# Kernel tuning notes

Measured on AMD Instinct MI355X. Metric: run time of the kernel, lower is better.

## Reference

```python
import jax, jax.numpy as jnp
import numpy as np

N_NODES = 1_000_000
N_EDGES = 16_000_000
D = 2          # num_dimensions (hard-coded in source)
H = 64         # hidden_channnels
G = 1024       # number of graphs in the batch


def setup_inputs() -> dict:
    key = jax.random.key(0)
    ks = jax.random.split(key, 10)
    x = jax.random.normal(ks[0], (N_NODES, D), dtype=jnp.float32)
    edge_index = jax.random.randint(ks[1], (2, N_EDGES), 0, N_NODES, dtype=jnp.int64)
    batch = jnp.sort(jax.random.randint(ks[2], (N_NODES,), 0, G, dtype=jnp.int64))
    s = 0.5
    return {
        "x": x,
        "lin_w": jax.random.normal(ks[3], (D, D), dtype=jnp.float32) * s,
        "lin_b": jnp.zeros((D,), jnp.float32),
        "gn_weight": jnp.ones((D,), jnp.float32),
        "gn_bias": jnp.zeros((D,), jnp.float32),
        "gn_mean_scale": jnp.ones((D,), jnp.float32),
        "gcn_w": jax.random.normal(ks[4], (D, D), dtype=jnp.float32) * s,
        "gcn_b": jnp.zeros((D,), jnp.float32),
        "fc1_w": jax.random.normal(ks[5], (H, D), dtype=jnp.float32) * s,
        "fc1_b": jnp.zeros((H,), jnp.float32),
        "fc2_w": jax.random.normal(ks[6], (D, H), dtype=jnp.float32) * (1.0 / np.sqrt(H)),
        "fc2_b": jnp.zeros((D,), jnp.float32),
        "edge_index": edge_index,
        "batch": batch,
    }


def reference(x, lin_w, lin_b, gn_weight, gn_bias, gn_mean_scale,
              gcn_w, gcn_b, fc1_w, fc1_b, fc2_w, fc2_b, edge_index, batch):
    n = x.shape[0]
    # lin
    h = x @ lin_w.T + lin_b
    # GraphNorm called without batch -> single-graph stats; eps = num_dimensions = 2 (arg-order quirk)
    mean = h.mean(axis=0)
    out = h - mean * gn_mean_scale
    var = (out * out).mean(axis=0)
    h = gn_weight * out * jax.lax.rsqrt(var + jnp.float32(D)) + gn_bias
    h = jax.nn.relu(h)
    # GCNConv (add_self_loops=True, sym norm) + residual
    row, col = edge_index[0], edge_index[1]
    deg = jax.ops.segment_sum(jnp.ones_like(col, dtype=h.dtype), col, num_segments=n) + 1.0
    dis = jax.lax.rsqrt(deg)                       # deg^{-1/2}
    hw = h @ gcn_w.T                               # [N, D]
    msg = (dis[row] * dis[col])[:, None] * hw[row] # [E, D]
    agg = jax.ops.segment_sum(msg, col, num_segments=n)
    conv = agg + hw / deg[:, None] + gcn_b         # self-loop term = dis_i^2 * hw_i
    h = conv + h
    # fc1
    h = h @ fc1_w.T + fc1_b                        # [N, H]
    # InstanceNorm1d on 2D input -> unbatched (C=N, L=H): per-row norm over H; eps = H (arg-order quirk)
    m = h.mean(axis=1, keepdims=True)
    v = ((h - m) ** 2).mean(axis=1, keepdims=True)
    h = (h - m) * jax.lax.rsqrt(v + jnp.float32(H))
    # fc2
    h = h @ fc2_w.T + fc2_b                        # [N, D]
    # scatter_mean over batch
    ssum = jax.ops.segment_sum(h, batch, num_segments=G)
    cnt = jax.ops.segment_sum(jnp.ones((n,), h.dtype), batch, num_segments=G)
    return ssum / jnp.maximum(cnt, 1.0)[:, None]
```

## Files before the change

kernel.cpp:

```cpp
#include <hip/hip_runtime.h>

#define BLK 256
#define CH 8192
#define BSHIFT 12
#define BRANGE 4096
#define BMASK 4095
#define NSB 512


__global__ void k_stats(const float* __restrict__ x, int n, double* __restrict__ partials) {
    float s0 = 0.f, s1 = 0.f, s2 = 0.f, s3 = 0.f, s4 = 0.f;
    int nv = n >> 1;
    int stride = gridDim.x * blockDim.x;
    for (int i = blockIdx.x * blockDim.x + threadIdx.x; i < nv; i += stride) {
        float4 v = reinterpret_cast<const float4*>(x)[i];
        s0 += v.x + v.z; s1 += v.y + v.w;
        s2 += v.x * v.x + v.z * v.z;
        s3 += v.y * v.y + v.w * v.w;
        s4 += v.x * v.y + v.z * v.w;
    }
    if (blockIdx.x == 0 && threadIdx.x == 0 && (n & 1)) {
        float2 v = reinterpret_cast<const float2*>(x)[n - 1];
        s0 += v.x; s1 += v.y; s2 += v.x * v.x; s3 += v.y * v.y; s4 += v.x * v.y;
    }
    for (int off = 32; off; off >>= 1) {
        s0 += __shfl_down(s0, off);
        s1 += __shfl_down(s1, off);
        s2 += __shfl_down(s2, off);
        s3 += __shfl_down(s3, off);
        s4 += __shfl_down(s4, off);
    }
    __shared__ double lds[4][5];
    int wid = threadIdx.x >> 6;
    if ((threadIdx.x & 63) == 0) {
        lds[wid][0] = s0; lds[wid][1] = s1; lds[wid][2] = s2;
        lds[wid][3] = s3; lds[wid][4] = s4;
    }
    __syncthreads();
    if (threadIdx.x == 0) {
        double t0 = 0, t1 = 0, t2 = 0, t3 = 0, t4 = 0;
        for (int w = 0; w < 4; ++w) {
            t0 += lds[w][0]; t1 += lds[w][1]; t2 += lds[w][2];
            t3 += lds[w][3]; t4 += lds[w][4];
        }
        double* o = partials + (size_t)blockIdx.x * 5;
        o[0] = t0; o[1] = t1; o[2] = t2; o[3] = t3; o[4] = t4;
    }
}


__global__ void k_params(const double* __restrict__ partials, int np,
                         const int* __restrict__ bhist, int NB,
                         int* __restrict__ gbase, int* __restrict__ cursor,
                         const float* lin_w, const float* lin_b,
                         const float* gn_w, const float* gn_b, const float* gn_ms,
                         const float* gcn_w, const float* gcn_b,
                         const float* fc1_w, const float* fc1_b,
                         const float* fc2_w, const float* fc2_b,
                         int n, float* __restrict__ P) {
    int tid = threadIdx.x;
    if (bhist) {
        __shared__ int si[256];
        int hv = (tid < NB) ? bhist[tid] : 0;
        si[tid] = hv; __syncthreads();
        for (int off = 1; off < 256; off <<= 1) {
            int t = (tid >= off) ? si[tid - off] : 0;
            __syncthreads();
            si[tid] += t;
            __syncthreads();
        }
        if (tid < NB) { gbase[tid] = si[tid] - hv; cursor[tid] = si[tid] - hv; }
        if (tid == 0) gbase[NB] = si[255];
        __syncthreads();
    }
    double a0 = 0, a1 = 0, a2 = 0, a3 = 0, a4 = 0;
    for (int i = tid; i < np; i += blockDim.x) {
        const double* q = partials + (size_t)i * 5;
        a0 += q[0]; a1 += q[1]; a2 += q[2]; a3 += q[3]; a4 += q[4];
    }
    for (int off = 32; off; off >>= 1) {
        a0 += __shfl_down(a0, off);
        a1 += __shfl_down(a1, off);
        a2 += __shfl_down(a2, off);
        a3 += __shfl_down(a3, off);
        a4 += __shfl_down(a4, off);
    }
    __shared__ double red[4][5];
    int wid = tid >> 6;
    if ((tid & 63) == 0) {
        red[wid][0] = a0; red[wid][1] = a1; red[wid][2] = a2;
        red[wid][3] = a3; red[wid][4] = a4;
    }
    __syncthreads();
    if (tid != 0) return;
    double Sx0 = 0, Sx1 = 0, Sxx = 0, Syy = 0, Sxy = 0;
    for (int w = 0; w < 4; ++w) {
        Sx0 += red[w][0]; Sx1 += red[w][1]; Sxx += red[w][2];
        Syy += red[w][3]; Sxy += red[w][4];
    }
    double N = (double)n;
    for (int c = 0; c < 2; ++c) {
        double L0 = lin_w[c * 2], L1 = lin_w[c * 2 + 1], lb = lin_b[c];
        double m   = (L0 * Sx0 + L1 * Sx1) / N + lb;
        double Eh2 = (L0 * L0 * Sxx + L1 * L1 * Syy + 2.0 * L0 * L1 * Sxy
                      + 2.0 * lb * (L0 * Sx0 + L1 * Sx1)) / N + lb * lb;
        double s   = gn_ms[c];
        double var = Eh2 - 2.0 * s * m * m + s * s * m * m;
        double inv = 1.0 / sqrt(var + 2.0);
        double gam = gn_w[c];
        P[c * 2 + 0] = (float)(gam * inv * L0);
        P[c * 2 + 1] = (float)(gam * inv * L1);
        P[4 + c]     = (float)(gam * inv * (lb - m * s) + gn_b[c]);
    }
    P[6] = gcn_w[0]; P[7] = gcn_w[1]; P[8] = gcn_w[2]; P[9] = gcn_w[3];
    P[10] = gcn_b[0]; P[11] = gcn_b[1];
    double b0 = 0, b1 = 0, bb = 0;
    for (int j = 0; j < 64; ++j) { b0 += fc1_w[2 * j]; b1 += fc1_w[2 * j + 1]; bb += fc1_b[j]; }
    b0 /= 64.0; b1 /= 64.0; bb /= 64.0;
    double S00 = 0, S01 = 0, S11 = 0, Sb0 = 0, Sb1 = 0, Sbb = 0;
    double M00 = 0, M01 = 0, M10 = 0, M11 = 0, t0 = 0, t1 = 0;
    for (int j = 0; j < 64; ++j) {
        double w0 = fc1_w[2 * j] - b0, w1 = fc1_w[2 * j + 1] - b1, b = fc1_b[j] - bb;
        S00 += w0 * w0; S01 += w0 * w1; S11 += w1 * w1;
        Sb0 += w0 * b;  Sb1 += w1 * b;  Sbb += b * b;
        double f0 = fc2_w[j], f1 = fc2_w[64 + j];
        M00 += f0 * w0; M01 += f0 * w1; t0 += f0 * b;
        M10 += f1 * w0; M11 += f1 * w1; t1 += f1 * b;
    }
    P[12] = (float)(S00 / 64.0); P[13] = (float)(S01 / 64.0); P[14] = (float)(S11 / 64.0);
    P[15] = (float)(Sb0 / 64.0); P[16] = (float)(Sb1 / 64.0); P[17] = (float)(Sbb / 64.0);
    P[18] = (float)M00; P[19] = (float)M01; P[20] = (float)M10; P[21] = (float)M11;
    P[22] = (float)t0;  P[23] = (float)t1;
    P[24] = fc2_b[0];   P[25] = fc2_b[1];
}


__global__ void k_hist(const int* __restrict__ col, int E, int NB, int* __restrict__ bhist) {
    __shared__ int h[256];
    for (int j = threadIdx.x; j < 256; j += blockDim.x) h[j] = 0;
    __syncthreads();
    int nq = E >> 2;
    int stride = gridDim.x * blockDim.x;
    for (int q = blockIdx.x * blockDim.x + threadIdx.x; q < nq; q += stride) {
        int4 c = reinterpret_cast<const int4*>(col)[q];
        atomicAdd(&h[c.x >> BSHIFT], 1);
        atomicAdd(&h[c.y >> BSHIFT], 1);
        atomicAdd(&h[c.z >> BSHIFT], 1);
        atomicAdd(&h[c.w >> BSHIFT], 1);
    }
    if (blockIdx.x == 0) {
        for (int e = (nq << 2) + threadIdx.x; e < E; e += blockDim.x)
            atomicAdd(&h[col[e] >> BSHIFT], 1);
    }
    __syncthreads();
    for (int j = threadIdx.x; j < NB; j += blockDim.x)
        if (h[j]) atomicAdd(&bhist[j], h[j]);
}

__global__ __launch_bounds__(256) void k_binA(const int* __restrict__ row,
                                              const int* __restrict__ col, int E,
                                              int NB, int* __restrict__ cursor,
                                              unsigned* __restrict__ staging) {
    __shared__ unsigned buf[CH];
    __shared__ int h[256], si[256], lpos[256], lcur[256];
    int tid = threadIdx.x;
    int start = blockIdx.x * CH;
    int end = start + CH; if (end > E) end = E;
    h[tid] = 0;
    __syncthreads();
    for (int e = start + tid; e < end; e += 256)
        atomicAdd(&h[col[e] >> BSHIFT], 1);
    __syncthreads();
    int hv = h[tid];
    si[tid] = hv; __syncthreads();
    for (int off = 1; off < 256; off <<= 1) {
        int t = (tid >= off) ? si[tid - off] : 0;
        __syncthreads();
        si[tid] += t;
        __syncthreads();
    }
    lpos[tid] = si[tid] - hv;
    lcur[tid] = (tid < NB && hv) ? atomicAdd(&cursor[tid], hv) : 0;
    __syncthreads();
    for (int e = start + tid; e < end; e += 256) {
        int c = col[e];
        unsigned w = ((unsigned)row[e] << BSHIFT) | (unsigned)(c & BMASK);
        int slot = atomicAdd(&lpos[c >> BSHIFT], 1);
        buf[slot] = w;
    }
    __syncthreads();
    int wid = tid >> 6, lane = tid & 63;
    for (int b = wid; b < NB; b += 4) {
        int m = h[b];
        if (!m) continue;
        int lb = si[b] - m;
        int g = lcur[b];
        for (int k = lane; k < m; k += 64)
            staging[g + k] = buf[lb + k];
    }
}

__global__ __launch_bounds__(1024) void k_degprep(const unsigned* __restrict__ staging,
                                                  const int* __restrict__ gbase,
                                                  const float* __restrict__ x,
                                                  const float* __restrict__ P,
                                                  int n, int* __restrict__ deg,
                                                  float2* __restrict__ p) {
    __shared__ int hist[BRANGE];
    int tid = threadIdx.x;
    for (int j = tid; j < BRANGE; j += 1024) hist[j] = 0;
    __syncthreads();
    int s = gbase[blockIdx.x], e = gbase[blockIdx.x + 1];
    int pre = (4 - (s & 3)) & 3; int cnt = e - s; if (pre > cnt) pre = cnt;
    for (int i = s + tid; i < s + pre; i += 1024)
        atomicAdd(&hist[staging[i] & BMASK], 1);
    int vs = s + pre;
    int nq = (e - vs) >> 2;
    const uint4* sv = reinterpret_cast<const uint4*>(staging + vs);
    for (int q = tid; q < nq; q += 1024) {
        uint4 w = sv[q];
        atomicAdd(&hist[w.x & BMASK], 1);
        atomicAdd(&hist[w.y & BMASK], 1);
        atomicAdd(&hist[w.z & BMASK], 1);
        atomicAdd(&hist[w.w & BMASK], 1);
    }
    for (int i = vs + (nq << 2) + tid; i < e; i += 1024)
        atomicAdd(&hist[staging[i] & BMASK], 1);
    __syncthreads();
    float A00 = P[0], A01 = P[1], A10 = P[2], A11 = P[3], q0 = P[4], q1 = P[5];
    float g00 = P[6], g01 = P[7], g10 = P[8], g11 = P[9];
    int nb = blockIdx.x << BSHIFT;
    int lim = n - nb; if (lim > BRANGE) lim = BRANGE;
    for (int j = tid; j < lim; j += 1024) {
        int d = hist[j];
        deg[nb + j] = d;
        float2 v = reinterpret_cast<const float2*>(x)[nb + j];
        float gg0 = fmaxf(fmaf(A00, v.x, fmaf(A01, v.y, q0)), 0.f);
        float gg1 = fmaxf(fmaf(A10, v.x, fmaf(A11, v.y, q1)), 0.f);
        float hw0 = g00 * gg0 + g01 * gg1;
        float hw1 = g10 * gg0 + g11 * gg1;
        float degf = (float)d + 1.0f;
        float dis = rsqrtf(degf);
        p[nb + j] = make_float2(dis * hw0, dis * hw1);
    }
}

__global__ void k_aggB(const unsigned* __restrict__ staging, const int* __restrict__ gbase,
                       const float2* __restrict__ p, int n, float2* __restrict__ agg) {
    __shared__ float acc[2 * BRANGE];
    for (int j = threadIdx.x; j < 2 * BRANGE; j += blockDim.x) acc[j] = 0.f;
    __syncthreads();
    int s = gbase[blockIdx.x], e = gbase[blockIdx.x + 1];
    int cnt = e - s;
    int pre = (4 - (s & 3)) & 3; if (pre > cnt) pre = cnt;
    for (int i = s + threadIdx.x; i < s + pre; i += blockDim.x) {
        unsigned w = staging[i]; float2 pv = p[w >> BSHIFT];
        atomicAdd(&acc[2 * (w & BMASK)],     pv.x);
        atomicAdd(&acc[2 * (w & BMASK) + 1], pv.y);
    }
    int vs = s + pre;
    int nq = (e - vs) >> 2;
    const uint4* sv = reinterpret_cast<const uint4*>(staging + vs);
    #pragma unroll 4
    for (int q = threadIdx.x; q < nq; q += blockDim.x) {
        uint4 w = sv[q];
        float2 p0 = p[w.x >> BSHIFT], p1 = p[w.y >> BSHIFT];
        float2 p2 = p[w.z >> BSHIFT], p3 = p[w.w >> BSHIFT];
        atomicAdd(&acc[2 * (w.x & BMASK)],     p0.x);
        atomicAdd(&acc[2 * (w.x & BMASK) + 1], p0.y);
        atomicAdd(&acc[2 * (w.y & BMASK)],     p1.x);
        atomicAdd(&acc[2 * (w.y & BMASK) + 1], p1.y);
        atomicAdd(&acc[2 * (w.z & BMASK)],     p2.x);
        atomicAdd(&acc[2 * (w.z & BMASK) + 1], p2.y);
        atomicAdd(&acc[2 * (w.w & BMASK)],     p3.x);
        atomicAdd(&acc[2 * (w.w & BMASK) + 1], p3.y);
    }
    for (int i = vs + (nq << 2) + threadIdx.x; i < e; i += blockDim.x) {
        unsigned w = staging[i]; float2 pv = p[w >> BSHIFT];
        atomicAdd(&acc[2 * (w & BMASK)],     pv.x);
        atomicAdd(&acc[2 * (w & BMASK) + 1], pv.y);
    }
    __syncthreads();
    int nb = blockIdx.x << BSHIFT;
    for (int j = threadIdx.x; j < BRANGE && nb + j < n; j += blockDim.x)
        agg[nb + j] = make_float2(acc[2 * j], acc[2 * j + 1]);
}


__global__ void k_final(const float* __restrict__ x, const int* __restrict__ deg,
                        const float* __restrict__ agg, const int* __restrict__ batch,
                        const float* __restrict__ P, int n,
                        float* __restrict__ gsum, float* __restrict__ gcnt) {
    int i = blockIdx.x * blockDim.x + threadIdx.x;
    bool valid = i < n;
    float A00 = P[0], A01 = P[1], A10 = P[2], A11 = P[3], q0 = P[4], q1 = P[5];
    float g00 = P[6], g01 = P[7], g10 = P[8], g11 = P[9];
    float gb0 = P[10], gb1 = P[11];
    float S00 = P[12], S01 = P[13], S11 = P[14], Sb0 = P[15], Sb1 = P[16], Sbb = P[17];
    float M00 = P[18], M01 = P[19], M10 = P[20], M11 = P[21];
    float t0 = P[22], t1 = P[23], fb0 = P[24], fb1 = P[25];

    float o0 = 0.f, o1 = 0.f;
    int b = 0;
    if (valid) {
        float2 v = reinterpret_cast<const float2*>(x)[i];
        float g0 = fmaxf(fmaf(A00, v.x, fmaf(A01, v.y, q0)), 0.f);
        float g1 = fmaxf(fmaf(A10, v.x, fmaf(A11, v.y, q1)), 0.f);
        float hw0 = g00 * g0 + g01 * g1;
        float hw1 = g10 * g0 + g11 * g1;
        float degf = (float)deg[i] + 1.0f;
        float dis = rsqrtf(degf);
        float a0 = agg[2 * i], a1 = agg[2 * i + 1];
        float c0 = dis * a0 + hw0 / degf + gb0 + g0;
        float c1 = dis * a1 + hw1 / degf + gb1 + g1;
        float vq = S00 * c0 * c0 + 2.f * S01 * c0 * c1 + S11 * c1 * c1
                 + 2.f * Sb0 * c0 + 2.f * Sb1 * c1 + Sbb;
        float inv = rsqrtf(vq + 64.0f);
        o0 = inv * (M00 * c0 + M01 * c1 + t0) + fb0;
        o1 = inv * (M10 * c0 + M11 * c1 + t1) + fb1;
        b = batch[i];
    }
    unsigned long long act = __ballot(valid);
    if (act == ~0ull) {
        int b0 = __shfl(b, 0);
        if (__all(b == b0)) {
            float s0 = o0, s1 = o1;
            for (int off = 32; off; off >>= 1) {
                s0 += __shfl_down(s0, off);
                s1 += __shfl_down(s1, off);
            }
            if ((threadIdx.x & 63) == 0) {
                atomicAdd(&gsum[2 * b0], s0);
                atomicAdd(&gsum[2 * b0 + 1], s1);
                atomicAdd(&gcnt[b0], 64.0f);
            }
        } else {
            atomicAdd(&gsum[2 * b], o0);
            atomicAdd(&gsum[2 * b + 1], o1);
            atomicAdd(&gcnt[b], 1.0f);
        }
    } else if (valid) {
        atomicAdd(&gsum[2 * b], o0);
        atomicAdd(&gsum[2 * b + 1], o1);
        atomicAdd(&gcnt[b], 1.0f);
    }
}

__global__ void k_div(const float* __restrict__ gsum, const float* __restrict__ gcnt,
                      float* __restrict__ out, int G) {
    int g = blockIdx.x * blockDim.x + threadIdx.x;
    if (g < G) {
        float c = fmaxf(gcnt[g], 1.0f);
        out[2 * g]     = gsum[2 * g] / c;
        out[2 * g + 1] = gsum[2 * g + 1] / c;
    }
}


__global__ void k_prep(const float* __restrict__ x, const int* __restrict__ deg,
                       const float* __restrict__ P, int n, float2* __restrict__ p) {
    int stride = gridDim.x * blockDim.x;
    float A00 = P[0], A01 = P[1], A10 = P[2], A11 = P[3], q0 = P[4], q1 = P[5];
    float g00 = P[6], g01 = P[7], g10 = P[8], g11 = P[9];
    for (int i = blockIdx.x * blockDim.x + threadIdx.x; i < n; i += stride) {
        float2 v = reinterpret_cast<const float2*>(x)[i];
        float g0 = fmaxf(fmaf(A00, v.x, fmaf(A01, v.y, q0)), 0.f);
        float g1 = fmaxf(fmaf(A10, v.x, fmaf(A11, v.y, q1)), 0.f);
        float hw0 = g00 * g0 + g01 * g1;
        float hw1 = g10 * g0 + g11 * g1;
        float degf = (float)deg[i] + 1.0f;
        float dis = rsqrtf(degf);
        p[i] = make_float2(dis * hw0, dis * hw1);
    }
}

__global__ void k_deg(const int* __restrict__ col, int E, int* __restrict__ deg) {
    int nq = (E + 3) >> 2;
    int q = blockIdx.x * blockDim.x + threadIdx.x;
    if (q >= nq) return;
    int base = q << 2;
    if (base + 3 < E) {
        int4 c = reinterpret_cast<const int4*>(col)[q];
        atomicAdd(&deg[c.x], 1); atomicAdd(&deg[c.y], 1);
        atomicAdd(&deg[c.z], 1); atomicAdd(&deg[c.w], 1);
    } else {
        for (int e = base; e < E; ++e) atomicAdd(&deg[col[e]], 1);
    }
}

__global__ void k_edge(const int* __restrict__ row, const int* __restrict__ col, int E,
                       const float2* __restrict__ p, float* __restrict__ agg) {
    int nq = (E + 3) >> 2;
    int q = blockIdx.x * blockDim.x + threadIdx.x;
    if (q >= nq) return;
    int base = q << 2;
    if (base + 3 < E) {
        int4 r = reinterpret_cast<const int4*>(row)[q];
        int4 c = reinterpret_cast<const int4*>(col)[q];
        float2 p0 = p[r.x], p1 = p[r.y], p2 = p[r.z], p3 = p[r.w];
        atomicAdd(&agg[2 * c.x], p0.x); atomicAdd(&agg[2 * c.x + 1], p0.y);
        atomicAdd(&agg[2 * c.y], p1.x); atomicAdd(&agg[2 * c.y + 1], p1.y);
        atomicAdd(&agg[2 * c.z], p2.x); atomicAdd(&agg[2 * c.z + 1], p2.y);
        atomicAdd(&agg[2 * c.w], p3.x); atomicAdd(&agg[2 * c.w + 1], p3.y);
    } else {
        for (int e = base; e < E; ++e) {
            float2 pv = p[row[e]];
            atomicAdd(&agg[2 * col[e]], pv.x);
            atomicAdd(&agg[2 * col[e] + 1], pv.y);
        }
    }
}


extern "C" void kernel_launch(void* const* d_in, const int* in_sizes, int n_in,
                              void* d_out, int out_size, void* d_ws, size_t ws_size,
                              hipStream_t stream) {
    const float* x      = (const float*)d_in[0];
    const float* lin_w  = (const float*)d_in[1];
    const float* lin_b  = (const float*)d_in[2];
    const float* gn_w   = (const float*)d_in[3];
    const float* gn_b   = (const float*)d_in[4];
    const float* gn_ms  = (const float*)d_in[5];
    const float* gcn_w  = (const float*)d_in[6];
    const float* gcn_b  = (const float*)d_in[7];
    const float* fc1_w  = (const float*)d_in[8];
    const float* fc1_b  = (const float*)d_in[9];
    const float* fc2_w  = (const float*)d_in[10];
    const float* fc2_b  = (const float*)d_in[11];
    const int*   ei     = (const int*)d_in[12];
    const int*   batch  = (const int*)d_in[13];

    int n = in_sizes[0] / 2;
    int E = in_sizes[12] / 2;
    int G = out_size / 2;
    const int* row = ei;
    const int* col = ei + E;

    char* ws = (char*)d_ws;
    int nb_nodes = (n + BLK - 1) / BLK;

    int NB = (n + BRANGE - 1) >> BSHIFT;

    size_t zero_end  = 16384 + (size_t)12 * G;
    size_t part_off  = (zero_end + 255) & ~(size_t)255;
    size_t deg_off   = (part_off + (size_t)40 * NSB + 255) & ~(size_t)255;
    size_t p_off     = deg_off + (size_t)4 * n;
    size_t agg_off   = p_off + (size_t)8 * n;
    size_t stag_off  = agg_off + (size_t)8 * n;
    size_t need      = stag_off + (size_t)4 * E;

    bool fast = (n <= (1 << 20)) && (NB <= 253) && (need <= ws_size) &&
                (zero_end <= 16384 + 12288);

    if (fast) {
        float*    P       = (float*)(ws + 64);
        int*      bhist   = (int*)(ws + 4096);
        int*      gbase   = (int*)(ws + 8192);
        int*      cursor  = (int*)(ws + 12288);
        float*    gsum    = (float*)(ws + 16384);
        float*    gcnt    = (float*)(ws + 16384 + (size_t)8 * G);
        double*   part    = (double*)(ws + part_off);
        int*      deg     = (int*)(ws + deg_off);
        float2*   p       = (float2*)(ws + p_off);
        float*    agg     = (float*)(ws + agg_off);
        unsigned* staging = (unsigned*)(ws + stag_off);

        hipMemsetAsync(d_ws, 0, zero_end, stream);

        int nbinA = (E + CH - 1) / CH;

        k_stats<<<NSB, BLK, 0, stream>>>(x, n, part);
        k_hist<<<512, BLK, 0, stream>>>(col, E, NB, bhist);
        k_params<<<1, 256, 0, stream>>>(part, NSB, bhist, NB, gbase, cursor,
                                        lin_w, lin_b, gn_w, gn_b, gn_ms,
                                        gcn_w, gcn_b, fc1_w, fc1_b, fc2_w, fc2_b, n, P);
        k_binA<<<nbinA, 256, 0, stream>>>(row, col, E, NB, cursor, staging);
        k_degprep<<<NB, 1024, 0, stream>>>(staging, gbase, x, P, n, deg, p);
        k_aggB<<<NB, 1024, 0, stream>>>(staging, gbase, p, n, (float2*)agg);
        k_final<<<nb_nodes, BLK, 0, stream>>>(x, deg, agg, batch, P, n, gsum, gcnt);
        k_div<<<(G + BLK - 1) / BLK, BLK, 0, stream>>>(gsum, gcnt, (float*)d_out, G);
    } else {
        float*  P     = (float*)(ws + 64);
        float*  gsum  = (float*)(ws + 4096);
        float*  gcnt  = (float*)(ws + 4096 + (size_t)8 * G);
        size_t fzero_end = 4096 + (size_t)12 * G;
        size_t fpart_off = (fzero_end + 255) & ~(size_t)255;
        size_t fdeg_off  = (fpart_off + (size_t)40 * NSB + 255) & ~(size_t)255;
        int*    deg   = (int*)(ws + fdeg_off);
        size_t fagg_off = fdeg_off + (size_t)4 * n;
        float*  agg   = (float*)(ws + fagg_off);
        size_t fp_off = fagg_off + (size_t)8 * n;
        float2* p     = (float2*)(ws + fp_off);
        double* part  = (double*)(ws + fpart_off);

        hipMemsetAsync(ws + 4096, 0, fzero_end - 4096, stream);
        hipMemsetAsync(ws + fdeg_off, 0, (size_t)12 * n, stream);

        int nq = (E + 3) >> 2;
        int nb_edge = (nq + BLK - 1) / BLK;

        k_stats<<<NSB, BLK, 0, stream>>>(x, n, part);
        k_deg<<<nb_edge, BLK, 0, stream>>>(col, E, deg);
        k_params<<<1, 256, 0, stream>>>(part, NSB, (const int*)nullptr, 0,
                                        (int*)nullptr, (int*)nullptr,
                                        lin_w, lin_b, gn_w, gn_b, gn_ms,
                                        gcn_w, gcn_b, fc1_w, fc1_b, fc2_w, fc2_b, n, P);
        k_prep<<<nb_nodes, BLK, 0, stream>>>(x, deg, P, n, p);
        k_edge<<<nb_edge, BLK, 0, stream>>>(row, col, E, p, agg);
        k_final<<<nb_nodes, BLK, 0, stream>>>(x, deg, agg, batch, P, n, gsum, gcnt);
        k_div<<<(G + BLK - 1) / BLK, BLK, 0, stream>>>(gsum, gcnt, (float*)d_out, G);
    }
}
```

Baseline: 401.9 us.

## Fuse aggregation with final epilogue and multi-pass source-range gather for cache locality

Merges the shared-memory aggregation kernel with the final per-node epilogue and graph scatter-mean. The agg array no longer makes a round trip through global memory, and one kernel launch is removed. The edge loop now runs several passes, each gathering only source rows in a ~2MB slice of p, so concurrent blocks hit a cache-resident window. The cost is that every pass re-reads the staging buffer (up to 8 times) and adds a branch per edge.

```diff
diff --git a/kernel.cpp b/kernel.cpp
--- a/kernel.cpp
+++ b/kernel.cpp
@@ -245,47 +245,191 @@
     }
 }
 
-__global__ void k_aggB(const unsigned* __restrict__ staging, const int* __restrict__ gbase,
-                       const float2* __restrict__ p, int n, float2* __restrict__ agg) {
+__global__ __launch_bounds__(1024) void k_aggfin(
+        const unsigned* __restrict__ staging, const int* __restrict__ gbase,
+        const float2* __restrict__ p, const float* __restrict__ x,
+        const int* __restrict__ deg, const int* __restrict__ batch,
+        const float* __restrict__ Pp, int n, int npass,
+        float* __restrict__ gsum, float* __restrict__ gcnt) {
     __shared__ float acc[2 * BRANGE];
-    for (int j = threadIdx.x; j < 2 * BRANGE; j += blockDim.x) acc[j] = 0.f;
+    int tid = threadIdx.x;
+    for (int j = tid; j < 2 * BRANGE; j += 1024) acc[j] = 0.f;
     __syncthreads();
     int s = gbase[blockIdx.x], e = gbase[blockIdx.x + 1];
     int cnt = e - s;
     int pre = (4 - (s & 3)) & 3; if (pre > cnt) pre = cnt;
-    for (int i = s + threadIdx.x; i < s + pre; i += blockDim.x) {
-        unsigned w = staging[i]; float2 pv = p[w >> BSHIFT];
-        atomicAdd(&acc[2 * (w & BMASK)],     pv.x);
-        atomicAdd(&acc[2 * (w & BMASK) + 1], pv.y);
-    }
     int vs = s + pre;
     int nq = (e - vs) >> 2;
     const uint4* sv = reinterpret_cast<const uint4*>(staging + vs);
-    #pragma unroll 4
-    for (int q = threadIdx.x; q < nq; q += blockDim.x) {
-        uint4 w = sv[q];
-        float2 p0 = p[w.x >> BSHIFT], p1 = p[w.y >> BSHIFT];
-        float2 p2 = p[w.z >> BSHIFT], p3 = p[w.w >> BSHIFT];
-        atomicAdd(&acc[2 * (w.x & BMASK)],     p0.x);
-        atomicAdd(&acc[2 * (w.x & BMASK) + 1], p0.y);
-        atomicAdd(&acc[2 * (w.y & BMASK)],     p1.x);
-        atomicAdd(&acc[2 * (w.y & BMASK) + 1], p1.y);
-        atomicAdd(&acc[2 * (w.z & BMASK)],     p2.x);
-        atomicAdd(&acc[2 * (w.z & BMASK) + 1], p2.y);
-        atomicAdd(&acc[2 * (w.w & BMASK)],     p3.x);
-        atomicAdd(&acc[2 * (w.w & BMASK) + 1], p3.y);
-    }
-    for (int i = vs + (nq << 2) + threadIdx.x; i < e; i += blockDim.x) {
-        unsigned w = staging[i]; float2 pv = p[w >> BSHIFT];
-        atomicAdd(&acc[2 * (w & BMASK)],     pv.x);
-        atomicAdd(&acc[2 * (w & BMASK) + 1], pv.y);
-    }
-    __syncthreads();
+    int tail = vs + (nq << 2);
+    unsigned qn = (unsigned)((n + npass - 1) / npass);
+
+    for (int pass = 0; pass < npass; ++pass) {
+        unsigned lo = (unsigned)pass * qn;
+        for (int i = s + tid; i < vs; i += 1024) {
+            unsigned w = staging[i];
+            unsigned r = w >> BSHIFT;
+            if (r - lo < qn) {
+                float2 pv = p[r];
+                atomicAdd(&acc[2 * (w & BMASK)],     pv.x);
+                atomicAdd(&acc[2 * (w & BMASK) + 1], pv.y);
+            }
+        }
+        #pragma unroll 2
+        for (int q = tid; q < nq; q += 1024) {
+            uint4 w = sv[q];
+            unsigned r0 = w.x >> BSHIFT, r1 = w.y >> BSHIFT;
+            unsigned r2 = w.z >> BSHIFT, r3 = w.w >> BSHIFT;
+            if (r0 - lo < qn) {
+                float2 pv = p[r0];
+                atomicAdd(&acc[2 * (w.x & BMASK)],     pv.x);
+                atomicAdd(&acc[2 * (w.x & BMASK) + 1], pv.y);
+            }
+            if (r1 - lo < qn) {
+                float2 pv = p[r1];
+                atomicAdd(&acc[2 * (w.y & BMASK)],     pv.x);
+                atomicAdd(&acc[2 * (w.y & BMASK) + 1], pv.y);
+            }
+            if (r2 - lo < qn) {
+                float2 pv = p[r2];
+                atomicAdd(&acc[2 * (w.z & BMASK)],     pv.x);
+                atomicAdd(&acc[2 * (w.z & BMASK) + 1], pv.y);
+            }
+            if (r3 - lo < qn) {
+                float2 pv = p[r3];
+                atomicAdd(&acc[2 * (w.w & BMASK)],     pv.x);
+                atomicAdd(&acc[2 * (w.w & BMASK) + 1], pv.y);
+            }
+        }
+        for (int i = tail + tid; i < e; i += 1024) {
+            unsigned w = staging[i];
+            unsigned r = w >> BSHIFT;
+            if (r - lo < qn) {
+                float2 pv = p[r];
+                atomicAdd(&acc[2 * (w & BMASK)],     pv.x);
+                atomicAdd(&acc[2 * (w & BMASK) + 1], pv.y);
+            }
+        }
+    }
+    __syncthreads();
+
+    float A00 = Pp[0], A01 = Pp[1], A10 = Pp[2], A11 = Pp[3], q0 = Pp[4], q1 = Pp[5];
+    float g00 = Pp[6], g01 = Pp[7], g10 = Pp[8], g11 = Pp[9];
+    float gb0 = Pp[10], gb1 = Pp[11];
+    float S00 = Pp[12], S01 = Pp[13], S11 = Pp[14], Sb0 = Pp[15], Sb1 = Pp[16], Sbb = Pp[17];
+    float M00 = Pp[18], M01 = Pp[19], M10 = Pp[20], M11 = Pp[21];
+    float t0 = Pp[22], t1 = Pp[23], fb0 = Pp[24], fb1 = Pp[25];
     int nb = blockIdx.x << BSHIFT;
-    for (int j = threadIdx.x; j < BRANGE && nb + j < n; j += blockDim.x)
-        agg[nb + j] = make_float2(acc[2 * j], acc[2 * j + 1]);
-}
-
+    int lim = n - nb; if (lim > BRANGE) lim = BRANGE;
+    for (int j = tid; j < lim; j += 1024) {
+        int i = nb + j;
+        float2 v = reinterpret_cast<const float2*>(x)[i];
+        float g0 = fmaxf(fmaf(A00, v.x, fmaf(A01, v.y, q0)), 0.f);
+        float g1 = fmaxf(fmaf(A10, v.x, fmaf(A11, v.y, q1)), 0.f);
+        float hw0 = g00 * g0 + g01 * g1;
+        float hw1 = g10 * g0 + g11 * g1;
+        float degf = (float)deg[i] + 1.0f;
+        float dis = rsqrtf(degf);
+        float a0 = acc[2 * j], a1 = acc[2 * j + 1];
+        float c0 = dis * a0 + hw0 / degf + gb0 + g0;
+        float c1 = dis * a1 + hw1 / degf + gb1 + g1;
+        float vq = S00 * c0 * c0 + 2.f * S01 * c0 * c1 + S11 * c1 * c1
+                 + 2.f * Sb0 * c0 + 2.f * Sb1 * c1 + Sbb;
+        float inv = rsqrtf(vq + 64.0f);
+        float o0 = inv * (M00 * c0 + M01 * c1 + t0) + fb0;
+        float o1 = inv * (M10 * c0 + M11 * c1 + t1) + fb1;
+        int b = batch[i];
+        unsigned long long act = __ballot(true);
+        if (act == ~0ull) {
+            int b0 = __shfl(b, 0);
+            if (__all(b == b0)) {
+                float s0 = o0, s1 = o1;
+                for (int off = 32; off; off >>= 1) {
+                    s0 += __shfl_down(s0, off);
+                    s1 += __shfl_down(s1, off);
+                }
+                if ((tid & 63) == 0) {
+                    atomicAdd(&gsum[2 * b0], s0);
+                    atomicAdd(&gsum[2 * b0 + 1], s1);
+                    atomicAdd(&gcnt[b0], 64.0f);
+                }
+            } else {
+                atomicAdd(&gsum[2 * b], o0);
+                atomicAdd(&gsum[2 * b + 1], o1);
+                atomicAdd(&gcnt[b], 1.0f);
+            }
+        } else {
+            atomicAdd(&gsum[2 * b], o0);
+            atomicAdd(&gsum[2 * b + 1], o1);
+            atomicAdd(&gcnt[b], 1.0f);
+        }
+    }
+}
+
+__global__ void k_div(const float* __restrict__ gsum, const float* __restrict__ gcnt,
+                      float* __restrict__ out, int G) {
+    int g = blockIdx.x * blockDim.x + threadIdx.x;
+    if (g < G) {
+        float c = fmaxf(gcnt[g], 1.0f);
+        out[2 * g]     = gsum[2 * g] / c;
+        out[2 * g + 1] = gsum[2 * g + 1] / c;
+    }
+}
+
+
+__global__ void k_prep(const float* __restrict__ x, const int* __restrict__ deg,
+                       const float* __restrict__ P, int n, float2* __restrict__ p) {
+    int stride = gridDim.x * blockDim.x;
+    float A00 = P[0], A01 = P[1], A10 = P[2], A11 = P[3], q0 = P[4], q1 = P[5];
+    float g00 = P[6], g01 = P[7], g10 = P[8], g11 = P[9];
+    for (int i = blockIdx.x * blockDim.x + threadIdx.x; i < n; i += stride) {
+        float2 v = reinterpret_cast<const float2*>(x)[i];
+        float g0 = fmaxf(fmaf(A00, v.x, fmaf(A01, v.y, q0)), 0.f);
+        float g1 = fmaxf(fmaf(A10, v.x, fmaf(A11, v.y, q1)), 0.f);
+        float hw0 = g00 * g0 + g01 * g1;
+        float hw1 = g10 * g0 + g11 * g1;
+        float degf = (float)deg[i] + 1.0f;
+        float dis = rsqrtf(degf);
+        p[i] = make_float2(dis * hw0, dis * hw1);
+    }
+}
+
+__global__ void k_deg(const int* __restrict__ col, int E, int* __restrict__ deg) {
+    int nq = (E + 3) >> 2;
+    int q = blockIdx.x * blockDim.x + threadIdx.x;
+    if (q >= nq) return;
+    int base = q << 2;
+    if (base + 3 < E) {
+        int4 c = reinterpret_cast<const int4*>(col)[q];
+        atomicAdd(&deg[c.x], 1); atomicAdd(&deg[c.y], 1);
+        atomicAdd(&deg[c.z], 1); atomicAdd(&deg[c.w], 1);
+    } else {
+        for (int e = base; e < E; ++e) atomicAdd(&deg[col[e]], 1);
+    }
+}
+
+__global__ void k_edge(const int* __restrict__ row, const int* __restrict__ col, int E,
+                       const float2* __restrict__ p, float* __restrict__ agg) {
+    int nq = (E + 3) >> 2;
+    int q = blockIdx.x * blockDim.x + threadIdx.x;
+    if (q >= nq) return;
+    int base = q << 2;
+    if (base + 3 < E) {
+        int4 r = reinterpret_cast<const int4*>(row)[q];
+        int4 c = reinterpret_cast<const int4*>(col)[q];
+        float2 p0 = p[r.x], p1 = p[r.y], p2 = p[r.z], p3 = p[r.w];
+        atomicAdd(&agg[2 * c.x], p0.x); atomicAdd(&agg[2 * c.x + 1], p0.y);
+        atomicAdd(&agg[2 * c.y], p1.x); atomicAdd(&agg[2 * c.y + 1], p1.y);
+        atomicAdd(&agg[2 * c.z], p2.x); atomicAdd(&agg[2 * c.z + 1], p2.y);
+        atomicAdd(&agg[2 * c.w], p3.x); atomicAdd(&agg[2 * c.w + 1], p3.y);
+    } else {
+        for (int e = base; e < E; ++e) {
+            float2 pv = p[row[e]];
+            atomicAdd(&agg[2 * col[e]], pv.x);
+            atomicAdd(&agg[2 * col[e] + 1], pv.y);
+        }
+    }
+}
 
 __global__ void k_final(const float* __restrict__ x, const int* __restrict__ deg,
                         const float* __restrict__ agg, const int* __restrict__ batch,
@@ -346,71 +490,6 @@
     }
 }
 
-__global__ void k_div(const float* __restrict__ gsum, const float* __restrict__ gcnt,
-                      float* __restrict__ out, int G) {
-    int g = blockIdx.x * blockDim.x + threadIdx.x;
-    if (g < G) {
-        float c = fmaxf(gcnt[g], 1.0f);
-        out[2 * g]     = gsum[2 * g] / c;
-        out[2 * g + 1] = gsum[2 * g + 1] / c;
-    }
-}
-
-
-__global__ void k_prep(const float* __restrict__ x, const int* __restrict__ deg,
-                       const float* __restrict__ P, int n, float2* __restrict__ p) {
-    int stride = gridDim.x * blockDim.x;
-    float A00 = P[0], A01 = P[1], A10 = P[2], A11 = P[3], q0 = P[4], q1 = P[5];
-    float g00 = P[6], g01 = P[7], g10 = P[8], g11 = P[9];
-    for (int i = blockIdx.x * blockDim.x + threadIdx.x; i < n; i += stride) {
-        float2 v = reinterpret_cast<const float2*>(x)[i];
-        float g0 = fmaxf(fmaf(A00, v.x, fmaf(A01, v.y, q0)), 0.f);
-        float g1 = fmaxf(fmaf(A10, v.x, fmaf(A11, v.y, q1)), 0.f);
-        float hw0 = g00 * g0 + g01 * g1;
-        float hw1 = g10 * g0 + g11 * g1;
-        float degf = (float)deg[i] + 1.0f;
-        float dis = rsqrtf(degf);
-        p[i] = make_float2(dis * hw0, dis * hw1);
-    }
-}
-
-__global__ void k_deg(const int* __restrict__ col, int E, int* __restrict__ deg) {
-    int nq = (E + 3) >> 2;
-    int q = blockIdx.x * blockDim.x + threadIdx.x;
-    if (q >= nq) return;
-    int base = q << 2;
-    if (base + 3 < E) {
-        int4 c = reinterpret_cast<const int4*>(col)[q];
-        atomicAdd(&deg[c.x], 1); atomicAdd(&deg[c.y], 1);
-        atomicAdd(&deg[c.z], 1); atomicAdd(&deg[c.w], 1);
-    } else {
-        for (int e = base; e < E; ++e) atomicAdd(&deg[col[e]], 1);
-    }
-}
-
-__global__ void k_edge(const int* __restrict__ row, const int* __restrict__ col, int E,
-                       const float2* __restrict__ p, float* __restrict__ agg) {
-    int nq = (E + 3) >> 2;
-    int q = blockIdx.x * blockDim.x + threadIdx.x;
-    if (q >= nq) return;
-    int base = q << 2;
-    if (base + 3 < E) {
-        int4 r = reinterpret_cast<const int4*>(row)[q];
-        int4 c = reinterpret_cast<const int4*>(col)[q];
-        float2 p0 = p[r.x], p1 = p[r.y], p2 = p[r.z], p3 = p[r.w];
-        atomicAdd(&agg[2 * c.x], p0.x); atomicAdd(&agg[2 * c.x + 1], p0.y);
-        atomicAdd(&agg[2 * c.y], p1.x); atomicAdd(&agg[2 * c.y + 1], p1.y);
-        atomicAdd(&agg[2 * c.z], p2.x); atomicAdd(&agg[2 * c.z + 1], p2.y);
-        atomicAdd(&agg[2 * c.w], p3.x); atomicAdd(&agg[2 * c.w + 1], p3.y);
-    } else {
-        for (int e = base; e < E; ++e) {
-            float2 pv = p[row[e]];
-            atomicAdd(&agg[2 * col[e]], pv.x);
-            atomicAdd(&agg[2 * col[e] + 1], pv.y);
-        }
-    }
-}
-
 
 extern "C" void kernel_launch(void* const* d_in, const int* in_sizes, int n_in,
                               void* d_out, int out_size, void* d_ws, size_t ws_size,
@@ -445,8 +524,7 @@
     size_t part_off  = (zero_end + 255) & ~(size_t)255;
     size_t deg_off   = (part_off + (size_t)40 * NSB + 255) & ~(size_t)255;
     size_t p_off     = deg_off + (size_t)4 * n;
-    size_t agg_off   = p_off + (size_t)8 * n;
-    size_t stag_off  = agg_off + (size_t)8 * n;
+    size_t stag_off  = p_off + (size_t)8 * n;
     size_t need      = stag_off + (size_t)4 * E;
 
     bool fast = (n <= (1 << 20)) && (NB <= 253) && (need <= ws_size) &&
@@ -462,12 +540,15 @@
         double*   part    = (double*)(ws + part_off);
         int*      deg     = (int*)(ws + deg_off);
         float2*   p       = (float2*)(ws + p_off);
-        float*    agg     = (float*)(ws + agg_off);
         unsigned* staging = (unsigned*)(ws + stag_off);
 
         hipMemsetAsync(d_ws, 0, zero_end, stream);
 
         int nbinA = (E + CH - 1) / CH;
+        size_t pbytes = (size_t)8 * n;
+        int npass = (int)((pbytes + (2u << 20) - 1) / (2u << 20));
+        if (npass < 1) npass = 1;
+        if (npass > 8) npass = 8;
 
         k_stats<<<NSB, BLK, 0, stream>>>(x, n, part);
         k_hist<<<512, BLK, 0, stream>>>(col, E, NB, bhist);
@@ -476,8 +557,8 @@
                                         gcn_w, gcn_b, fc1_w, fc1_b, fc2_w, fc2_b, n, P);
         k_binA<<<nbinA, 256, 0, stream>>>(row, col, E, NB, cursor, staging);
         k_degprep<<<NB, 1024, 0, stream>>>(staging, gbase, x, P, n, deg, p);
-        k_aggB<<<NB, 1024, 0, stream>>>(staging, gbase, p, n, (float2*)agg);
-        k_final<<<nb_nodes, BLK, 0, stream>>>(x, deg, agg, batch, P, n, gsum, gcnt);
+        k_aggfin<<<NB, 1024, 0, stream>>>(staging, gbase, p, x, deg, batch,
+                                          P, n, npass, gsum, gcnt);
         k_div<<<(G + BLK - 1) / BLK, BLK, 0, stream>>>(gsum, gcnt, (float*)d_out, G);
     } else {
         float*  P     = (float*)(ws + 64);
```

Measured after the change: 378.8 us. 5.8% less time.

## Split per-bucket degree/aggregation across blocks and fuse final epilogue into aggregation

Applied to the files above, without the earlier changes.

Each destination bucket's degree histogram and aggregation is now split across multiple blocks (2 and 4 by default). Partial results go to global scratch, and the last-arriving block, found via an atomic counter, reduces them. The aggregation kernel also absorbs the former k_final epilogue, so the agg array never round-trips through global memory. This targets low occupancy with only ~245 buckets on a large GPU, at the cost of extra partial-buffer traffic and threadfence/counter synchronisation.

```diff
diff --git a/kernel.cpp b/kernel.cpp
--- a/kernel.cpp
+++ b/kernel.cpp
@@ -204,32 +204,46 @@
                                                   const int* __restrict__ gbase,
                                                   const float* __restrict__ x,
                                                   const float* __restrict__ P,
-                                                  int n, int* __restrict__ deg,
+                                                  int n, int split,
+                                                  int* __restrict__ phist,
+                                                  int* __restrict__ cntD,
+                                                  int* __restrict__ deg,
                                                   float2* __restrict__ p) {
     __shared__ int hist[BRANGE];
+    __shared__ int lastflag;
     int tid = threadIdx.x;
+    int b  = blockIdx.x / split;
+    int sl = blockIdx.x % split;
     for (int j = tid; j < BRANGE; j += 1024) hist[j] = 0;
     __syncthreads();
-    int s = gbase[blockIdx.x], e = gbase[blockIdx.x + 1];
-    int pre = (4 - (s & 3)) & 3; int cnt = e - s; if (pre > cnt) pre = cnt;
-    for (int i = s + tid; i < s + pre; i += 1024)
+    int s = gbase[b], e = gbase[b + 1];
+    int cnt = e - s;
+    int qper = (cnt + split - 1) / split;
+    int i0 = s + sl * qper;
+    int i1 = i0 + qper; if (i1 > e) i1 = e;
+    for (int i = i0 + tid; i < i1; i += 1024)
         atomicAdd(&hist[staging[i] & BMASK], 1);
-    int vs = s + pre;
-    int nq = (e - vs) >> 2;
-    const uint4* sv = reinterpret_cast<const uint4*>(staging + vs);
-    for (int q = tid; q < nq; q += 1024) {
-        uint4 w = sv[q];
-        atomicAdd(&hist[w.x & BMASK], 1);
-        atomicAdd(&hist[w.y & BMASK], 1);
-        atomicAdd(&hist[w.z & BMASK], 1);
-        atomicAdd(&hist[w.w & BMASK], 1);
-    }
-    for (int i = vs + (nq << 2) + tid; i < e; i += 1024)
-        atomicAdd(&hist[staging[i] & BMASK], 1);
-    __syncthreads();
+    __syncthreads();
+
+    if (split > 1) {
+        int* ph = phist + ((size_t)b * split + sl) * BRANGE;
+        for (int j = tid; j < BRANGE; j += 1024) ph[j] = hist[j];
+        __threadfence();
+        if (tid == 0) lastflag = atomicAdd(&cntD[b], 1);
+        __syncthreads();
+        if (lastflag != split - 1) return;
+        __threadfence();
+        for (int o = 0; o < split; ++o) {
+            if (o == sl) continue;
+            const int* po = phist + ((size_t)b * split + o) * BRANGE;
+            for (int j = tid; j < BRANGE; j += 1024) hist[j] += po[j];
+        }
+        __syncthreads();
+    }
+
     float A00 = P[0], A01 = P[1], A10 = P[2], A11 = P[3], q0 = P[4], q1 = P[5];
     float g00 = P[6], g01 = P[7], g10 = P[8], g11 = P[9];
-    int nb = blockIdx.x << BSHIFT;
+    int nb = b << BSHIFT;
     int lim = n - nb; if (lim > BRANGE) lim = BRANGE;
     for (int j = tid; j < lim; j += 1024) {
         int d = hist[j];
@@ -245,24 +259,36 @@
     }
 }
 
-__global__ void k_aggB(const unsigned* __restrict__ staging, const int* __restrict__ gbase,
-                       const float2* __restrict__ p, int n, float2* __restrict__ agg) {
+__global__ __launch_bounds__(512) void k_aggfin(
+        const unsigned* __restrict__ staging, const int* __restrict__ gbase,
+        const float2* __restrict__ p, const float* __restrict__ x,
+        const int* __restrict__ deg, const int* __restrict__ batch,
+        const float* __restrict__ Pp, int n, int split,
+        float* __restrict__ pacc, int* __restrict__ cntA,
+        float* __restrict__ gsum, float* __restrict__ gcnt) {
     __shared__ float acc[2 * BRANGE];
-    for (int j = threadIdx.x; j < 2 * BRANGE; j += blockDim.x) acc[j] = 0.f;
-    __syncthreads();
-    int s = gbase[blockIdx.x], e = gbase[blockIdx.x + 1];
-    int cnt = e - s;
-    int pre = (4 - (s & 3)) & 3; if (pre > cnt) pre = cnt;
-    for (int i = s + threadIdx.x; i < s + pre; i += blockDim.x) {
-        unsigned w = staging[i]; float2 pv = p[w >> BSHIFT];
-        atomicAdd(&acc[2 * (w & BMASK)],     pv.x);
-        atomicAdd(&acc[2 * (w & BMASK) + 1], pv.y);
-    }
-    int vs = s + pre;
-    int nq = (e - vs) >> 2;
-    const uint4* sv = reinterpret_cast<const uint4*>(staging + vs);
-    #pragma unroll 4
-    for (int q = threadIdx.x; q < nq; q += blockDim.x) {
+    __shared__ int lastflag;
+    int tid = threadIdx.x;
+    int b  = blockIdx.x / split;
+    int sl = blockIdx.x % split;
+    for (int j = tid; j < 2 * BRANGE; j += 512) acc[j] = 0.f;
+    __syncthreads();
+    int s = gbase[b], e = gbase[b + 1];
+    int a0 = (s + 3) & ~3; if (a0 > e) a0 = e;
+    if (sl == 0) {
+        for (int i = s + tid; i < a0; i += 512) {
+            unsigned w = staging[i]; float2 pv = p[w >> BSHIFT];
+            atomicAdd(&acc[2 * (w & BMASK)],     pv.x);
+            atomicAdd(&acc[2 * (w & BMASK) + 1], pv.y);
+        }
+    }
+    int nq = (e - a0) >> 2; if (nq < 0) nq = 0;
+    const uint4* sv = reinterpret_cast<const uint4*>(staging + a0);
+    int qper = (nq + split - 1) / split;
+    int q0 = sl * qper;
+    int q1 = q0 + qper; if (q1 > nq) q1 = nq;
+    #pragma unroll 2
+    for (int q = q0 + tid; q < q1; q += 512) {
         uint4 w = sv[q];
         float2 p0 = p[w.x >> BSHIFT], p1 = p[w.y >> BSHIFT];
         float2 p2 = p[w.z >> BSHIFT], p3 = p[w.w >> BSHIFT];
@@ -275,17 +301,144 @@
         atomicAdd(&acc[2 * (w.w & BMASK)],     p3.x);
         atomicAdd(&acc[2 * (w.w & BMASK) + 1], p3.y);
     }
-    for (int i = vs + (nq << 2) + threadIdx.x; i < e; i += blockDim.x) {
-        unsigned w = staging[i]; float2 pv = p[w >> BSHIFT];
-        atomicAdd(&acc[2 * (w & BMASK)],     pv.x);
-        atomicAdd(&acc[2 * (w & BMASK) + 1], pv.y);
-    }
-    __syncthreads();
-    int nb = blockIdx.x << BSHIFT;
-    for (int j = threadIdx.x; j < BRANGE && nb + j < n; j += blockDim.x)
-        agg[nb + j] = make_float2(acc[2 * j], acc[2 * j + 1]);
-}
-
+    if (sl == split - 1) {
+        for (int i = a0 + (nq << 2) + tid; i < e; i += 512) {
+            unsigned w = staging[i]; float2 pv = p[w >> BSHIFT];
+            atomicAdd(&acc[2 * (w & BMASK)],     pv.x);
+            atomicAdd(&acc[2 * (w & BMASK) + 1], pv.y);
+        }
+    }
+    __syncthreads();
+
+    if (split > 1) {
+        float* pa = pacc + ((size_t)b * split + sl) * (2 * BRANGE);
+        for (int j = tid; j < 2 * BRANGE; j += 512) pa[j] = acc[j];
+        __threadfence();
+        if (tid == 0) lastflag = atomicAdd(&cntA[b], 1);
+        __syncthreads();
+        if (lastflag != split - 1) return;
+        __threadfence();
+        for (int j = tid; j < 2 * BRANGE; j += 512) {
+            float v = acc[j];
+            for (int o = 0; o < split; ++o) {
+                if (o == sl) continue;
+                v += pacc[((size_t)b * split + o) * (2 * BRANGE) + j];
+            }
+            acc[j] = v;
+        }
+        __syncthreads();
+    }
+
+    float A00 = Pp[0], A01 = Pp[1], A10 = Pp[2], A11 = Pp[3], q0f = Pp[4], q1f = Pp[5];
+    float g00 = Pp[6], g01 = Pp[7], g10 = Pp[8], g11 = Pp[9];
+    float gb0 = Pp[10], gb1 = Pp[11];
+    float S00 = Pp[12], S01 = Pp[13], S11 = Pp[14], Sb0 = Pp[15], Sb1 = Pp[16], Sbb = Pp[17];
+    float M00 = Pp[18], M01 = Pp[19], M10 = Pp[20], M11 = Pp[21];
+    float t0 = Pp[22], t1 = Pp[23], fb0 = Pp[24], fb1 = Pp[25];
+    int nb = b << BSHIFT;
+    int lim = n - nb; if (lim > BRANGE) lim = BRANGE;
+    for (int j = tid; j < lim; j += 512) {
+        int i = nb + j;
+        float2 v = reinterpret_cast<const float2*>(x)[i];
+        float g0 = fmaxf(fmaf(A00, v.x, fmaf(A01, v.y, q0f)), 0.f);
+        float g1 = fmaxf(fmaf(A10, v.x, fmaf(A11, v.y, q1f)), 0.f);
+        float hw0 = g00 * g0 + g01 * g1;
+        float hw1 = g10 * g0 + g11 * g1;
+        float degf = (float)deg[i] + 1.0f;
+        float dis = rsqrtf(degf);
+        float a0v = acc[2 * j], a1v = acc[2 * j + 1];
+        float c0 = dis * a0v + hw0 / degf + gb0 + g0;
+        float c1 = dis * a1v + hw1 / degf + gb1 + g1;
+        float vq = S00 * c0 * c0 + 2.f * S01 * c0 * c1 + S11 * c1 * c1
+                 + 2.f * Sb0 * c0 + 2.f * Sb1 * c1 + Sbb;
+        float inv = rsqrtf(vq + 64.0f);
+        float o0 = inv * (M00 * c0 + M01 * c1 + t0) + fb0;
+        float o1 = inv * (M10 * c0 + M11 * c1 + t1) + fb1;
+        int bg = batch[i];
+        int b0 = __shfl(bg, 0);
+        if (__all(bg == b0)) {
+            float s0 = o0, s1 = o1;
+            for (int off = 32; off; off >>= 1) {
+                s0 += __shfl_down(s0, off);
+                s1 += __shfl_down(s1, off);
+            }
+            if ((tid & 63) == 0) {
+                atomicAdd(&gsum[2 * b0], s0);
+                atomicAdd(&gsum[2 * b0 + 1], s1);
+                atomicAdd(&gcnt[b0], 64.0f);
+            }
+        } else {
+            atomicAdd(&gsum[2 * bg], o0);
+            atomicAdd(&gsum[2 * bg + 1], o1);
+            atomicAdd(&gcnt[bg], 1.0f);
+        }
+    }
+}
+
+__global__ void k_div(const float* __restrict__ gsum, const float* __restrict__ gcnt,
+                      float* __restrict__ out, int G) {
+    int g = blockIdx.x * blockDim.x + threadIdx.x;
+    if (g < G) {
+        float c = fmaxf(gcnt[g], 1.0f);
+        out[2 * g]     = gsum[2 * g] / c;
+        out[2 * g + 1] = gsum[2 * g + 1] / c;
+    }
+}
+
+
+__global__ void k_prep(const float* __restrict__ x, const int* __restrict__ deg,
+                       const float* __restrict__ P, int n, float2* __restrict__ p) {
+    int stride = gridDim.x * blockDim.x;
+    float A00 = P[0], A01 = P[1], A10 = P[2], A11 = P[3], q0 = P[4], q1 = P[5];
+    float g00 = P[6], g01 = P[7], g10 = P[8], g11 = P[9];
+    for (int i = blockIdx.x * blockDim.x + threadIdx.x; i < n; i += stride) {
+        float2 v = reinterpret_cast<const float2*>(x)[i];
+        float g0 = fmaxf(fmaf(A00, v.x, fmaf(A01, v.y, q0)), 0.f);
+        float g1 = fmaxf(fmaf(A10, v.x, fmaf(A11, v.y, q1)), 0.f);
+        float hw0 = g00 * g0 + g01 * g1;
+        float hw1 = g10 * g0 + g11 * g1;
+        float degf = (float)deg[i] + 1.0f;
+        float dis = rsqrtf(degf);
+        p[i] = make_float2(dis * hw0, dis * hw1);
+    }
+}
+
+__global__ void k_deg(const int* __restrict__ col, int E, int* __restrict__ deg) {
+    int nq = (E + 3) >> 2;
+    int q = blockIdx.x * blockDim.x + threadIdx.x;
+    if (q >= nq) return;
+    int base = q << 2;
+    if (base + 3 < E) {
+        int4 c = reinterpret_cast<const int4*>(col)[q];
+        atomicAdd(&deg[c.x], 1); atomicAdd(&deg[c.y], 1);
+        atomicAdd(&deg[c.z], 1); atomicAdd(&deg[c.w], 1);
+    } else {
+        for (int e = base; e < E; ++e) atomicAdd(&deg[col[e]], 1);
+    }
+}
+
+__global__ void k_edge(const int* __restrict__ row, const int* __restrict__ col, int E,
+                       const float2* __restrict__ p, float* __restrict__ agg) {
+    int nq = (E + 3) >> 2;
+    int q = blockIdx.x * blockDim.x + threadIdx.x;
+    if (q >= nq) return;
+    int base = q << 2;
+    if (base + 3 < E) {
+        int4 r = reinterpret_cast<const int4*>(row)[q];
+        int4 c = reinterpret_cast<const int4*>(col)[q];
+        float2 p0 = p[r.x], p1 = p[r.y], p2 = p[r.z], p3 = p[r.w];
+        atomicAdd(&agg[2 * c.x], p0.x); atomicAdd(&agg[2 * c.x + 1], p0.y);
+        atomicAdd(&agg[2 * c.y], p1.x); atomicAdd(&agg[2 * c.y + 1], p1.y);
+        atomicAdd(&agg[2 * c.z], p2.x); atomicAdd(&agg[2 * c.z + 1], p2.y);
+        atomicAdd(&agg[2 * c.w], p3.x); atomicAdd(&agg[2 * c.w + 1], p3.y);
+    } else {
+        for (int e = base; e < E; ++e) {
+            float2 pv = p[row[e]];
+            atomicAdd(&agg[2 * col[e]], pv.x);
+            atomicAdd(&agg[2 * col[e] + 1], pv.y);
+        }
+    }
+}
 
 __global__ void k_final(const float* __restrict__ x, const int* __restrict__ deg,
                         const float* __restrict__ agg, const int* __restrict__ batch,
@@ -346,71 +499,6 @@
     }
 }
 
-__global__ void k_div(const float* __restrict__ gsum, const float* __restrict__ gcnt,
-                      float* __restrict__ out, int G) {
-    int g = blockIdx.x * blockDim.x + threadIdx.x;
-    if (g < G) {
-        float c = fmaxf(gcnt[g], 1.0f);
-        out[2 * g]     = gsum[2 * g] / c;
-        out[2 * g + 1] = gsum[2 * g + 1] / c;
-    }
-}
-
-
-__global__ void k_prep(const float* __restrict__ x, const int* __restrict__ deg,
-                       const float* __restrict__ P, int n, float2* __restrict__ p) {
-    int stride = gridDim.x * blockDim.x;
-    float A00 = P[0], A01 = P[1], A10 = P[2], A11 = P[3], q0 = P[4], q1 = P[5];
-    float g00 = P[6], g01 = P[7], g10 = P[8], g11 = P[9];
-    for (int i = blockIdx.x * blockDim.x + threadIdx.x; i < n; i += stride) {
-        float2 v = reinterpret_cast<const float2*>(x)[i];
-        float g0 = fmaxf(fmaf(A00, v.x, fmaf(A01, v.y, q0)), 0.f);
-        float g1 = fmaxf(fmaf(A10, v.x, fmaf(A11, v.y, q1)), 0.f);
-        float hw0 = g00 * g0 + g01 * g1;
-        float hw1 = g10 * g0 + g11 * g1;
-        float degf = (float)deg[i] + 1.0f;
-        float dis = rsqrtf(degf);
-        p[i] = make_float2(dis * hw0, dis * hw1);
-    }
-}
-
-__global__ void k_deg(const int* __restrict__ col, int E, int* __restrict__ deg) {
-    int nq = (E + 3) >> 2;
-    int q = blockIdx.x * blockDim.x + threadIdx.x;
-    if (q >= nq) return;
-    int base = q << 2;
-    if (base + 3 < E) {
-        int4 c = reinterpret_cast<const int4*>(col)[q];
-        atomicAdd(&deg[c.x], 1); atomicAdd(&deg[c.y], 1);
-        atomicAdd(&deg[c.z], 1); atomicAdd(&deg[c.w], 1);
-    } else {
-        for (int e = base; e < E; ++e) atomicAdd(&deg[col[e]], 1);
-    }
-}
-
-__global__ void k_edge(const int* __restrict__ row, const int* __restrict__ col, int E,
-                       const float2* __restrict__ p, float* __restrict__ agg) {
-    int nq = (E + 3) >> 2;
-    int q = blockIdx.x * blockDim.x + threadIdx.x;
-    if (q >= nq) return;
-    int base = q << 2;
-    if (base + 3 < E) {
-        int4 r = reinterpret_cast<const int4*>(row)[q];
-        int4 c = reinterpret_cast<const int4*>(col)[q];
-        float2 p0 = p[r.x], p1 = p[r.y], p2 = p[r.z], p3 = p[r.w];
-        atomicAdd(&agg[2 * c.x], p0.x); atomicAdd(&agg[2 * c.x + 1], p0.y);
-        atomicAdd(&agg[2 * c.y], p1.x); atomicAdd(&agg[2 * c.y + 1], p1.y);
-        atomicAdd(&agg[2 * c.z], p2.x); atomicAdd(&agg[2 * c.z + 1], p2.y);
-        atomicAdd(&agg[2 * c.w], p3.x); atomicAdd(&agg[2 * c.w + 1], p3.y);
-    } else {
-        for (int e = base; e < E; ++e) {
-            float2 pv = p[row[e]];
-            atomicAdd(&agg[2 * col[e]], pv.x);
-            atomicAdd(&agg[2 * col[e] + 1], pv.y);
-        }
-    }
-}
-
 
 extern "C" void kernel_launch(void* const* d_in, const int* in_sizes, int n_in,
                               void* d_out, int out_size, void* d_ws, size_t ws_size,
@@ -438,19 +526,27 @@
 
     char* ws = (char*)d_ws;
     int nb_nodes = (n + BLK - 1) / BLK;
-
     int NB = (n + BRANGE - 1) >> BSHIFT;
 
-    size_t zero_end  = 16384 + (size_t)12 * G;
-    size_t part_off  = (zero_end + 255) & ~(size_t)255;
-    size_t deg_off   = (part_off + (size_t)40 * NSB + 255) & ~(size_t)255;
-    size_t p_off     = deg_off + (size_t)4 * n;
-    size_t agg_off   = p_off + (size_t)8 * n;
-    size_t stag_off  = agg_off + (size_t)8 * n;
-    size_t need      = stag_off + (size_t)4 * E;
+    int splitA = 4, splitD = 2;
+    size_t zero_end = 0, part_off = 0, deg_off = 0, p_off = 0,
+           phist_off = 0, pacc_off = 0, stag_off = 0, need = 0;
+    const int cand[4][2] = {{4, 2}, {2, 2}, {2, 1}, {1, 1}};
+    for (int ci = 0; ci < 4; ++ci) {
+        splitA = cand[ci][0]; splitD = cand[ci][1];
+        zero_end  = 16384 + (size_t)12 * G + 2048;
+        part_off  = (zero_end + 255) & ~(size_t)255;
+        deg_off   = (part_off + (size_t)40 * NSB + 255) & ~(size_t)255;
+        p_off     = deg_off + (size_t)4 * n;
+        phist_off = p_off + (size_t)8 * n;
+        pacc_off  = phist_off + (splitD > 1 ? (size_t)NB * splitD * BRANGE * 4 : 0);
+        stag_off  = pacc_off + (splitA > 1 ? (size_t)NB * splitA * 2 * BRANGE * 4 : 0);
+        need      = stag_off + (size_t)4 * E;
+        if (need <= ws_size) break;
+    }
 
     bool fast = (n <= (1 << 20)) && (NB <= 253) && (need <= ws_size) &&
-                (zero_end <= 16384 + 12288);
+                ((size_t)(16384 + 12 * G + 2048) <= 16384 + 12288 + 2048);
 
     if (fast) {
         float*    P       = (float*)(ws + 64);
@@ -459,10 +555,13 @@
         int*      cursor  = (int*)(ws + 12288);
         float*    gsum    = (float*)(ws + 16384);
         float*    gcnt    = (float*)(ws + 16384 + (size_t)8 * G);
+        int*      cntD    = (int*)(ws + 16384 + (size_t)12 * G);
+        int*      cntA    = (int*)(ws + 16384 + (size_t)12 * G + 1024);
         double*   part    = (double*)(ws + part_off);
         int*      deg     = (int*)(ws + deg_off);
         float2*   p       = (float2*)(ws + p_off);
-        float*    agg     = (float*)(ws + agg_off);
+        int*      phist   = (int*)(ws + phist_off);
+        float*    pacc    = (float*)(ws + pacc_off);
         unsigned* staging = (unsigned*)(ws + stag_off);
 
         hipMemsetAsync(d_ws, 0, zero_end, stream);
@@ -475,9 +574,10 @@
                                         lin_w, lin_b, gn_w, gn_b, gn_ms,
                                         gcn_w, gcn_b, fc1_w, fc1_b, fc2_w, fc2_b, n, P);
         k_binA<<<nbinA, 256, 0, stream>>>(row, col, E, NB, cursor, staging);
-        k_degprep<<<NB, 1024, 0, stream>>>(staging, gbase, x, P, n, deg, p);
-        k_aggB<<<NB, 1024, 0, stream>>>(staging, gbase, p, n, (float2*)agg);
-        k_final<<<nb_nodes, BLK, 0, stream>>>(x, deg, agg, batch, P, n, gsum, gcnt);
+        k_degprep<<<NB * splitD, 1024, 0, stream>>>(staging, gbase, x, P, n, splitD,
+                                                    phist, cntD, deg, p);
+        k_aggfin<<<NB * splitA, 512, 0, stream>>>(staging, gbase, p, x, deg, batch,
+                                                  P, n, splitA, pacc, cntA, gsum, gcnt);
         k_div<<<(G + BLK - 1) / BLK, BLK, 0, stream>>>(gsum, gcnt, (float*)d_out, G);
     } else {
         float*  P     = (float*)(ws + 64);
```

New measurement: 1.085 ms. 170% more time.
